# Performance work log

Measured on AMD Instinct MI355X. Metric: run time of the kernel, lower is better.

Reference implementation:

```python
import jax, jax.numpy as jnp
import numpy as np

B, HI, WI, DIM = 16, 64, 64, 256
HEADS, HEAD_DIM, NUM_MEM = 8, 32, 4
HID = HEADS * HEAD_DIM


def setup_inputs() -> dict:
    key = jax.random.key(0)
    ks = jax.random.split(key, 6)
    return {
        "x": jax.random.normal(ks[0], (B, HI, WI, DIM), jnp.float32),
        "gamma_in": jax.random.normal(ks[1], (DIM,), jnp.float32) * 0.02,
        "w_qkv": jax.random.normal(ks[2], (DIM, 3 * HID), jnp.float32) / np.sqrt(DIM),
        "b_qkv": jnp.zeros((3 * HID,), jnp.float32),
        "mem_kv": jax.random.normal(ks[3], (2, HEADS, NUM_MEM, HEAD_DIM), jnp.float32),
        "w_out": jax.random.normal(ks[4], (HID, DIM), jnp.float32) / np.sqrt(HID),
        "b_out": jnp.zeros((DIM,), jnp.float32),
        "gamma_out": jax.random.normal(ks[5], (DIM,), jnp.float32) * 0.02,
    }


def reference(x, gamma_in, w_qkv, b_qkv, mem_kv, w_out, b_out, gamma_out):
    b, h, w, c = x.shape
    n = h * w
    rms_scale = c ** 0.5
    attn_scale = HEAD_DIM ** -0.5

    # RMSNorm (as written in source: pure learned scaling)
    xn = x * (gamma_in + 1.0) * rms_scale

    # 1x1 conv == per-pixel linear projection
    qkv = xn @ w_qkv + b_qkv                       # (b, h, w, 3*HID)
    q, k, v = jnp.split(qkv, 3, axis=-1)

    def to_heads(t):                                # (b,h,w,HID) -> (b, heads, d, n)
        return t.reshape(b, n, HEADS, HEAD_DIM).transpose(0, 2, 3, 1)

    q, k, v = map(to_heads, (q, k, v))

    # memory kv: (heads, m, d) -> (b, heads, d, m), concat along sequence axis
    mk = jnp.broadcast_to(mem_kv[0].transpose(0, 2, 1)[None], (b, HEADS, HEAD_DIM, NUM_MEM))
    mv = jnp.broadcast_to(mem_kv[1].transpose(0, 2, 1)[None], (b, HEADS, HEAD_DIM, NUM_MEM))
    k = jnp.concatenate([mk, k], axis=-1)           # (b, heads, d, n+m)
    v = jnp.concatenate([mv, v], axis=-1)

    # feature-map attention: softmax q over feature dim, k over sequence dim
    q = jax.nn.softmax(q * attn_scale, axis=-2)     # source scales q before softmax
    k = jax.nn.softmax(k, axis=-1)

    context = jnp.einsum('bhdn,bhen->bhde', k, v)   # (b, heads, d, e) small
    out = jnp.einsum('bhde,bhdn->bhen', context, q) # (b, heads, e, n)

    out = out.transpose(0, 3, 1, 2).reshape(b, h, w, HID)
    y = out @ w_out + b_out                         # 1x1 output conv
    return y * (gamma_out + 1.0) * rms_scale        # output RMSNorm
```

## Files before the change

kernel.cpp:

```cpp
#include <hip/hip_runtime.h>
#include <hip/hip_bf16.h>

typedef __bf16 bf16_t;
typedef _Float16 fp16_t;
typedef _Float16 f16x8 __attribute__((ext_vector_type(8)));
typedef __bf16 bf16x8 __attribute__((ext_vector_type(8)));
typedef __bf16 bf16x4 __attribute__((ext_vector_type(4)));
typedef float f32x4 __attribute__((ext_vector_type(4)));

#define ATTN_SCALE 0.17677669529663687f
#define K_SHIFT 64.0f
#define Q_SHIFT 8.0f

__device__ __forceinline__ void gload16(const void* g, void* l) {
  __builtin_amdgcn_global_load_lds((const __attribute__((address_space(1))) void*)g,
                                   (__attribute__((address_space(3))) void*)l, 16, 0, 0);
}

__global__ __launch_bounds__(256) void prep_pack(
    const float* __restrict__ w_qkv, fp16_t* __restrict__ Bpack) {
  int idx = blockIdx.x * 256 + threadIdx.x;
  int l = idx & 63;
  int rest = idx >> 6;
  int f = rest & 3;
  int kk = (rest >> 2) & 7;
  int nt = rest >> 5;
  int n = nt * 64 + f * 16 + (l & 15);
  int k0 = kk * 32 + (l >> 4) * 8;
  f16x8 v;
#pragma unroll
  for (int e = 0; e < 8; ++e) v[e] = (fp16_t)w_qkv[(k0 + e) * 768 + n];
  ((f16x8*)Bpack)[idx] = v;
}

__global__ __launch_bounds__(256) void gemm_qvk_ctx(
    const float* __restrict__ x, const float* __restrict__ gamma_in,
    const fp16_t* __restrict__ Bpack, const float* __restrict__ bias,
    fp16_t* __restrict__ qe_out, float* __restrict__ part) {
  __shared__ fp16_t A[64 * 256];
  __shared__ bf16_t Pl[64 * 64];
  __shared__ bf16_t Vl[64 * 64];
  int t = threadIdx.x, l = t & 63, w = t >> 6;
  int lr = l >> 4, lc = l & 15;
  int bx = blockIdx.x;
  int m0 = bx * 64;

#pragma unroll
  for (int i = 0; i < 8; ++i) {
    int idx = i * 256 + t;
    int r = idx >> 5, c8 = idx & 31;
    const float* src = x + (size_t)(m0 + r) * 256 + c8 * 8;
    const float* gsc = gamma_in + c8 * 8;
    f16x8 hv;
#pragma unroll
    for (int j = 0; j < 8; ++j) hv[j] = (fp16_t)(src[j] * (gsc[j] + 1.f) * 16.f);
    *(f16x8*)&A[r * 256 + ((c8 ^ (r & 31)) * 8)] = hv;
  }
  __syncthreads();

  {
    const fp16_t* Bp = Bpack + (size_t)w * 16384;
    f32x4 acc[4][4];
#pragma unroll
    for (int mf = 0; mf < 4; ++mf)
#pragma unroll
      for (int nf = 0; nf < 4; ++nf) acc[mf][nf] = (f32x4){0.f, 0.f, 0.f, 0.f};
#pragma unroll
    for (int kk = 0; kk < 8; ++kk) {
      f16x8 af[4], bfr[4];
#pragma unroll
      for (int f = 0; f < 4; ++f) {
        int ra = f * 16 + lc;
        af[f] = *(const f16x8*)&A[ra * 256 + (((kk * 4 + lr) ^ (ra & 31)) * 8)];
        bfr[f] = *(const f16x8*)(Bp + (size_t)(kk * 4 + f) * 512 + l * 8);
      }
#pragma unroll
      for (int mf = 0; mf < 4; ++mf)
#pragma unroll
        for (int nf = 0; nf < 4; ++nf)
          acc[mf][nf] = __builtin_amdgcn_mfma_f32_16x16x32_f16(af[mf], bfr[nf], acc[mf][nf], 0, 0, 0);
    }
    int n0 = w * 64;
    float bq[4];
#pragma unroll
    for (int nf = 0; nf < 4; ++nf) bq[nf] = bias[n0 + nf * 16 + lc];
#pragma unroll
    for (int mf = 0; mf < 4; ++mf)
#pragma unroll
      for (int r = 0; r < 4; ++r) {
        int row = m0 + mf * 16 + lr * 4 + r;
#pragma unroll
        for (int nf = 0; nf < 4; ++nf) {
          float ql = (acc[mf][nf][r] + bq[nf]) * ATTN_SCALE;
          qe_out[(size_t)row * 256 + n0 + nf * 16 + lc] = (fp16_t)__expf(ql - Q_SHIFT);
        }
      }
  }

  bool isK = (w < 2);
  int rh = w & 1;
  int hq = w & 1;
  int chalf = w >> 1;
  for (int ph = 0; ph < 4; ++ph) {
    int nt = (isK ? 4 : 8) + ph;
    const fp16_t* Bp = Bpack + (size_t)nt * 16384;
    f32x4 acc[2][4];
#pragma unroll
    for (int mf = 0; mf < 2; ++mf)
#pragma unroll
      for (int nf = 0; nf < 4; ++nf) acc[mf][nf] = (f32x4){0.f, 0.f, 0.f, 0.f};
#pragma unroll
    for (int kk = 0; kk < 8; ++kk) {
      f16x8 af[2], bfr[4];
#pragma unroll
      for (int f = 0; f < 2; ++f) {
        int ra = rh * 32 + f * 16 + lc;
        af[f] = *(const f16x8*)&A[ra * 256 + (((kk * 4 + lr) ^ (ra & 31)) * 8)];
      }
#pragma unroll
      for (int f = 0; f < 4; ++f)
        bfr[f] = *(const f16x8*)(Bp + (size_t)(kk * 4 + f) * 512 + l * 8);
#pragma unroll
      for (int mf = 0; mf < 2; ++mf)
#pragma unroll
        for (int nf = 0; nf < 4; ++nf)
          acc[mf][nf] = __builtin_amdgcn_mfma_f32_16x16x32_f16(af[mf], bfr[nf], acc[mf][nf], 0, 0, 0);
    }
    int n0 = nt * 64;
    float bv[4];
#pragma unroll
    for (int nf = 0; nf < 4; ++nf) bv[nf] = bias[n0 + nf * 16 + lc];
#pragma unroll
    for (int mf = 0; mf < 2; ++mf) {
#pragma unroll
      for (int nf = 0; nf < 4; ++nf) {
        int col = nf * 16 + lc;
        int row0 = rh * 32 + mf * 16 + lr * 4;
        bf16x4 pk;
#pragma unroll
        for (int r = 0; r < 4; ++r) {
          float val = acc[mf][nf][r] + bv[nf];
          pk[r] = isK ? (bf16_t)__expf(val - K_SHIFT) : (bf16_t)val;
        }
        int addr = col * 64 + ((((row0 >> 3) ^ (col & 7)) << 3) | (row0 & 7));
        if (isK) *(bf16x4*)&Pl[addr] = pk;
        else     *(bf16x4*)&Vl[addr] = pk;
      }
    }
    __syncthreads();

    {
      int hb = hq * 32;
      f32x4 sacc[2];
      f32x4 zacc[2];
#pragma unroll
      for (int mf = 0; mf < 2; ++mf) {
        sacc[mf] = (f32x4){0.f, 0.f, 0.f, 0.f};
        zacc[mf] = (f32x4){0.f, 0.f, 0.f, 0.f};
      }
      bf16x8 ones;
#pragma unroll
      for (int i = 0; i < 8; ++i) ones[i] = (bf16_t)1.0f;
#pragma unroll
      for (int kk = 0; kk < 2; ++kk) {
        bf16x8 ap[2], bvv;
#pragma unroll
        for (int mf = 0; mf < 2; ++mf) {
          int colA = hb + mf * 16 + lc;
          ap[mf] = *(const bf16x8*)&Pl[colA * 64 + (((kk * 4 + lr) ^ (colA & 7)) << 3)];
        }
        int colB = hb + chalf * 16 + lc;
        bvv = *(const bf16x8*)&Vl[colB * 64 + (((kk * 4 + lr) ^ (colB & 7)) << 3)];
#pragma unroll
        for (int mf = 0; mf < 2; ++mf) {
          sacc[mf] = __builtin_amdgcn_mfma_f32_16x16x32_bf16(ap[mf], bvv, sacc[mf], 0, 0, 0);
          if (chalf == 0)
            zacc[mf] = __builtin_amdgcn_mfma_f32_16x16x32_bf16(ap[mf], ones, zacc[mf], 0, 0, 0);
        }
      }
      float* pp = part + (size_t)bx * 8448 + (ph * 2 + hq) * 1056;
#pragma unroll
      for (int mf = 0; mf < 2; ++mf)
#pragma unroll
        for (int r = 0; r < 4; ++r) {
          int dd = mf * 16 + lr * 4 + r;
          pp[dd * 32 + chalf * 16 + lc] = sacc[mf][r];
          if (chalf == 0 && lc == 0) pp[1024 + dd] = zacc[mf][r];
        }
    }
    __syncthreads();
  }
}

__global__ __launch_bounds__(256) void build_wt(
    const float* __restrict__ part, const float* __restrict__ w_out,
    const float* __restrict__ mem_kv, fp16_t* __restrict__ Bpacky) {
  int bh = blockIdx.x;
  int b = bh >> 3, h = bh & 7;
  int t = threadIdx.x;
  __shared__ float S[32][32];
  __shared__ float Zr[32];
  __shared__ float W[32][256];
  for (int idx = t; idx < 1024; idx += 256) {
    float s = 0.f;
    for (int c = 0; c < 64; ++c) s += part[((size_t)(b * 64 + c)) * 8448 + h * 1056 + idx];
    S[idx >> 5][idx & 31] = s;
  }
  if (t < 32) {
    float zz = 0.f;
    for (int c = 0; c < 64; ++c) zz += part[((size_t)(b * 64 + c)) * 8448 + h * 1056 + 1024 + t];
    Zr[t] = zz;
  }
  for (int i = t; i < 32 * 256; i += 256) W[i >> 8][i & 255] = w_out[(h * 32 + (i >> 8)) * 256 + (i & 255)];
  __syncthreads();
  if (t < 32) {
    int dd = t;
    for (int m = 0; m < 4; ++m) {
      float p = __expf(mem_kv[h * 128 + m * 32 + dd] - K_SHIFT);
      Zr[dd] += p;
      for (int e = 0; e < 32; ++e) S[dd][e] += p * mem_kv[1024 + h * 128 + m * 32 + e];
    }
  }
  __syncthreads();
  int c = t;
  int nt = c >> 6, f = (c >> 4) & 3, lc = c & 15;
  for (int dd = 0; dd < 32; ++dd) {
    float acc = 0;
#pragma unroll 8
    for (int e = 0; e < 32; ++e) acc += S[dd][e] * W[e][c];
    int kcol = h * 32 + dd;
    int kk = kcol >> 5, lr = (kcol & 31) >> 3, e8 = kcol & 7;
    size_t addr = ((((size_t)(b * 4 + nt) * 8 + kk) * 4 + f) * 64 + (lr * 16 + lc)) * 8 + e8;
    Bpacky[addr] = (fp16_t)(acc / Zr[dd]);
  }
}

__global__ __launch_bounds__(256) void gemm_y(
    const fp16_t* __restrict__ qe, const fp16_t* __restrict__ Bpacky,
    const float* __restrict__ b_out, const float* __restrict__ gamma_out,
    float* __restrict__ y_out) {
  __shared__ fp16_t A[64 * 256];
  __shared__ float zbuf[64][8];
  int t = threadIdx.x, l = t & 63, w = t >> 6;
  int lr = l >> 4, lc = l & 15;
  int m0 = blockIdx.x * 64;
#pragma unroll
  for (int i = 0; i < 8; ++i) {
    int idx = i * 256 + t;
    int r = idx >> 5, cs = idx & 31;
    gload16(qe + (size_t)(m0 + r) * 256 + ((cs ^ (r & 31)) * 8), &A[idx * 8]);
  }
  __syncthreads();

#pragma unroll
  for (int pi = 0; pi < 2; ++pi) {
    int p = pi * 256 + t;
    int r = p >> 3, hh = p & 7;
    float zs = 0.f;
#pragma unroll
    for (int c = 0; c < 4; ++c) {
      int cs = (hh * 4 + c) ^ (r & 31);
      f16x8 vv = *(const f16x8*)&A[r * 256 + cs * 8];
#pragma unroll
      for (int j = 0; j < 8; ++j) zs += (float)vv[j];
    }
    zbuf[r][hh] = 1.f / zs;
  }
  __syncthreads();

#pragma unroll
  for (int i = 0; i < 8; ++i) {
    int idx = i * 256 + t;
    int r = idx >> 5, cs = idx & 31;
    int hh = (cs ^ (r & 31)) >> 2;
    float sc = zbuf[r][hh];
    f16x8 vv = *(const f16x8*)&A[idx * 8];
#pragma unroll
    for (int j = 0; j < 8; ++j) vv[j] = (fp16_t)((float)vv[j] * sc);
    *(f16x8*)&A[idx * 8] = vv;
  }
  __syncthreads();

  int n0 = w * 64;
  const fp16_t* Bp = Bpacky + (size_t)(m0 >> 12) * 65536 + (size_t)w * 16384;
  f32x4 acc[4][4];
#pragma unroll
  for (int mf = 0; mf < 4; ++mf)
#pragma unroll
    for (int nf = 0; nf < 4; ++nf) acc[mf][nf] = (f32x4){0.f, 0.f, 0.f, 0.f};
#pragma unroll
  for (int kk = 0; kk < 8; ++kk) {
    f16x8 af[4], bfr[4];
#pragma unroll
    for (int f = 0; f < 4; ++f) {
      int ra = f * 16 + lc;
      af[f] = *(const f16x8*)&A[ra * 256 + (((kk * 4 + lr) ^ (ra & 31)) * 8)];
      bfr[f] = *(const f16x8*)(Bp + (size_t)(kk * 4 + f) * 512 + l * 8);
    }
#pragma unroll
    for (int mf = 0; mf < 4; ++mf)
#pragma unroll
      for (int nf = 0; nf < 4; ++nf)
        acc[mf][nf] = __builtin_amdgcn_mfma_f32_16x16x32_f16(af[mf], bfr[nf], acc[mf][nf], 0, 0, 0);
  }
  float bv[4], gv[4];
#pragma unroll
  for (int nf = 0; nf < 4; ++nf) {
    int c = n0 + nf * 16 + lc;
    bv[nf] = b_out[c];
    gv[nf] = (gamma_out[c] + 1.f) * 16.f;
  }
#pragma unroll
  for (int mf = 0; mf < 4; ++mf)
#pragma unroll
    for (int r = 0; r < 4; ++r) {
      int row = m0 + mf * 16 + lr * 4 + r;
#pragma unroll
      for (int nf = 0; nf < 4; ++nf)
        y_out[(size_t)row * 256 + n0 + nf * 16 + lc] = (acc[mf][nf][r] + bv[nf]) * gv[nf];
    }
}

extern "C" void kernel_launch(void* const* d_in, const int* in_sizes, int n_in,
                              void* d_out, int out_size, void* d_ws, size_t ws_size,
                              hipStream_t stream) {
  const float* x        = (const float*)d_in[0];
  const float* gamma_in = (const float*)d_in[1];
  const float* w_qkv    = (const float*)d_in[2];
  const float* b_qkv    = (const float*)d_in[3];
  const float* mem_kv   = (const float*)d_in[4];
  const float* w_out    = (const float*)d_in[5];
  const float* b_out    = (const float*)d_in[6];
  const float* gamma_out= (const float*)d_in[7];
  float* y = (float*)d_out;

  char* ws = (char*)d_ws;
  fp16_t* qe     = (fp16_t*)(ws);
  fp16_t* Bpack  = (fp16_t*)(ws + 33554432);
  fp16_t* Bpacky = (fp16_t*)(ws + 33947648);
  float*  part   = (float*)(ws + 36044800);

  prep_pack<<<96, 256, 0, stream>>>(w_qkv, Bpack);
  gemm_qvk_ctx<<<1024, 256, 0, stream>>>(x, gamma_in, Bpack, b_qkv, qe, part);
  build_wt<<<128, 256, 0, stream>>>(part, w_out, mem_kv, Bpacky);
  gemm_y<<<1024, 256, 0, stream>>>(qe, Bpacky, b_out, gamma_out, y);
}
```

Before: 128.1 us.

## Recompute Q projection in output GEMM instead of storing exp(q) intermediate

Moves the Q projection out of the KV/context kernel into the final output kernel. There it recomputes Q from x, applies a proper per-head softmax with wave shuffles, and feeds the result straight from LDS into the y GEMM. This removes the 32 MB fp16 qe write and read round trip and the separate normalization passes. The cost is reading x twice, once in each kernel, plus redoing the Q GEMM in the second kernel.

```diff
diff --git a/kernel.cpp b/kernel.cpp
--- a/kernel.cpp
+++ b/kernel.cpp
@@ -10,7 +10,6 @@
 
 #define ATTN_SCALE 0.17677669529663687f
 #define K_SHIFT 64.0f
-#define Q_SHIFT 8.0f
 
 __device__ __forceinline__ void gload16(const void* g, void* l) {
   __builtin_amdgcn_global_load_lds((const __attribute__((address_space(1))) void*)g,
@@ -33,10 +32,10 @@
   ((f16x8*)Bpack)[idx] = v;
 }
 
-__global__ __launch_bounds__(256) void gemm_qvk_ctx(
+__global__ __launch_bounds__(256) void gemm_kv_ctx(
     const float* __restrict__ x, const float* __restrict__ gamma_in,
     const fp16_t* __restrict__ Bpack, const float* __restrict__ bias,
-    fp16_t* __restrict__ qe_out, float* __restrict__ part) {
+    float* __restrict__ part) {
   __shared__ fp16_t A[64 * 256];
   __shared__ bf16_t Pl[64 * 64];
   __shared__ bf16_t Vl[64 * 64];
@@ -57,45 +56,6 @@
     *(f16x8*)&A[r * 256 + ((c8 ^ (r & 31)) * 8)] = hv;
   }
   __syncthreads();
-
-  {
-    const fp16_t* Bp = Bpack + (size_t)w * 16384;
-    f32x4 acc[4][4];
-#pragma unroll
-    for (int mf = 0; mf < 4; ++mf)
-#pragma unroll
-      for (int nf = 0; nf < 4; ++nf) acc[mf][nf] = (f32x4){0.f, 0.f, 0.f, 0.f};
-#pragma unroll
-    for (int kk = 0; kk < 8; ++kk) {
-      f16x8 af[4], bfr[4];
-#pragma unroll
-      for (int f = 0; f < 4; ++f) {
-        int ra = f * 16 + lc;
-        af[f] = *(const f16x8*)&A[ra * 256 + (((kk * 4 + lr) ^ (ra & 31)) * 8)];
-        bfr[f] = *(const f16x8*)(Bp + (size_t)(kk * 4 + f) * 512 + l * 8);
-      }
-#pragma unroll
-      for (int mf = 0; mf < 4; ++mf)
-#pragma unroll
-        for (int nf = 0; nf < 4; ++nf)
-          acc[mf][nf] = __builtin_amdgcn_mfma_f32_16x16x32_f16(af[mf], bfr[nf], acc[mf][nf], 0, 0, 0);
-    }
-    int n0 = w * 64;
-    float bq[4];
-#pragma unroll
-    for (int nf = 0; nf < 4; ++nf) bq[nf] = bias[n0 + nf * 16 + lc];
-#pragma unroll
-    for (int mf = 0; mf < 4; ++mf)
-#pragma unroll
-      for (int r = 0; r < 4; ++r) {
-        int row = m0 + mf * 16 + lr * 4 + r;
-#pragma unroll
-        for (int nf = 0; nf < 4; ++nf) {
-          float ql = (acc[mf][nf][r] + bq[nf]) * ATTN_SCALE;
-          qe_out[(size_t)row * 256 + n0 + nf * 16 + lc] = (fp16_t)__expf(ql - Q_SHIFT);
-        }
-      }
-  }
 
   bool isK = (w < 2);
   int rh = w & 1;
@@ -235,55 +195,97 @@
   }
 }
 
-__global__ __launch_bounds__(256) void gemm_y(
-    const fp16_t* __restrict__ qe, const fp16_t* __restrict__ Bpacky,
+__global__ __launch_bounds__(256) void gemm_qy(
+    const float* __restrict__ x, const float* __restrict__ gamma_in,
+    const fp16_t* __restrict__ Bpack, const float* __restrict__ bias,
+    const fp16_t* __restrict__ Bpacky,
     const float* __restrict__ b_out, const float* __restrict__ gamma_out,
     float* __restrict__ y_out) {
   __shared__ fp16_t A[64 * 256];
-  __shared__ float zbuf[64][8];
   int t = threadIdx.x, l = t & 63, w = t >> 6;
   int lr = l >> 4, lc = l & 15;
   int m0 = blockIdx.x * 64;
+
 #pragma unroll
   for (int i = 0; i < 8; ++i) {
     int idx = i * 256 + t;
-    int r = idx >> 5, cs = idx & 31;
-    gload16(qe + (size_t)(m0 + r) * 256 + ((cs ^ (r & 31)) * 8), &A[idx * 8]);
-  }
-  __syncthreads();
-
-#pragma unroll
-  for (int pi = 0; pi < 2; ++pi) {
-    int p = pi * 256 + t;
-    int r = p >> 3, hh = p & 7;
-    float zs = 0.f;
-#pragma unroll
-    for (int c = 0; c < 4; ++c) {
-      int cs = (hh * 4 + c) ^ (r & 31);
-      f16x8 vv = *(const f16x8*)&A[r * 256 + cs * 8];
-#pragma unroll
-      for (int j = 0; j < 8; ++j) zs += (float)vv[j];
-    }
-    zbuf[r][hh] = 1.f / zs;
-  }
-  __syncthreads();
-
-#pragma unroll
-  for (int i = 0; i < 8; ++i) {
-    int idx = i * 256 + t;
-    int r = idx >> 5, cs = idx & 31;
-    int hh = (cs ^ (r & 31)) >> 2;
-    float sc = zbuf[r][hh];
-    f16x8 vv = *(const f16x8*)&A[idx * 8];
-#pragma unroll
-    for (int j = 0; j < 8; ++j) vv[j] = (fp16_t)((float)vv[j] * sc);
-    *(f16x8*)&A[idx * 8] = vv;
-  }
-  __syncthreads();
-
-  int n0 = w * 64;
+    int r = idx >> 5, c8 = idx & 31;
+    const float* src = x + (size_t)(m0 + r) * 256 + c8 * 8;
+    const float* gsc = gamma_in + c8 * 8;
+    f16x8 hv;
+#pragma unroll
+    for (int j = 0; j < 8; ++j) hv[j] = (fp16_t)(src[j] * (gsc[j] + 1.f) * 16.f);
+    *(f16x8*)&A[r * 256 + ((c8 ^ (r & 31)) * 8)] = hv;
+  }
+  __syncthreads();
+
+  f32x4 acc[4][4];
+#pragma unroll
+  for (int mf = 0; mf < 4; ++mf)
+#pragma unroll
+    for (int nf = 0; nf < 4; ++nf) acc[mf][nf] = (f32x4){0.f, 0.f, 0.f, 0.f};
+  {
+    const fp16_t* Bp = Bpack + (size_t)w * 16384;
+#pragma unroll
+    for (int kk = 0; kk < 8; ++kk) {
+      f16x8 af[4], bfr[4];
+#pragma unroll
+      for (int f = 0; f < 4; ++f) {
+        int ra = f * 16 + lc;
+        af[f] = *(const f16x8*)&A[ra * 256 + (((kk * 4 + lr) ^ (ra & 31)) * 8)];
+        bfr[f] = *(const f16x8*)(Bp + (size_t)(kk * 4 + f) * 512 + l * 8);
+      }
+#pragma unroll
+      for (int mf = 0; mf < 4; ++mf)
+#pragma unroll
+        for (int nf = 0; nf < 4; ++nf)
+          acc[mf][nf] = __builtin_amdgcn_mfma_f32_16x16x32_f16(af[mf], bfr[nf], acc[mf][nf], 0, 0, 0);
+    }
+  }
+  __syncthreads();
+
+  {
+    int n0 = w * 64;
+    float bq[4];
+#pragma unroll
+    for (int nf = 0; nf < 4; ++nf) bq[nf] = bias[n0 + nf * 16 + lc];
+#pragma unroll
+    for (int mf = 0; mf < 4; ++mf) {
+#pragma unroll
+      for (int r = 0; r < 4; ++r) {
+        int row = mf * 16 + lr * 4 + r;
+        float v0 = (acc[mf][0][r] + bq[0]) * ATTN_SCALE;
+        float v1 = (acc[mf][1][r] + bq[1]) * ATTN_SCALE;
+        float v2 = (acc[mf][2][r] + bq[2]) * ATTN_SCALE;
+        float v3 = (acc[mf][3][r] + bq[3]) * ATTN_SCALE;
+        float mA = fmaxf(v0, v1), mB = fmaxf(v2, v3);
+#pragma unroll
+        for (int s = 1; s < 16; s <<= 1) {
+          mA = fmaxf(mA, __shfl_xor(mA, s));
+          mB = fmaxf(mB, __shfl_xor(mB, s));
+        }
+        float e0 = __expf(v0 - mA), e1 = __expf(v1 - mA);
+        float e2 = __expf(v2 - mB), e3 = __expf(v3 - mB);
+        float sA = e0 + e1, sB = e2 + e3;
+#pragma unroll
+        for (int s = 1; s < 16; s <<= 1) {
+          sA += __shfl_xor(sA, s);
+          sB += __shfl_xor(sB, s);
+        }
+        float rA = 1.f / sA, rB = 1.f / sB;
+        float qv[4] = {e0 * rA, e1 * rA, e2 * rB, e3 * rB};
+#pragma unroll
+        for (int nf = 0; nf < 4; ++nf) {
+          int col = n0 + nf * 16 + lc;
+          int c8 = col >> 3;
+          A[row * 256 + ((c8 ^ (row & 31)) * 8) + (col & 7)] = (fp16_t)qv[nf];
+        }
+      }
+    }
+  }
+  __syncthreads();
+
   const fp16_t* Bp = Bpacky + (size_t)(m0 >> 12) * 65536 + (size_t)w * 16384;
-  f32x4 acc[4][4];
 #pragma unroll
   for (int mf = 0; mf < 4; ++mf)
 #pragma unroll
@@ -303,6 +305,7 @@
       for (int nf = 0; nf < 4; ++nf)
         acc[mf][nf] = __builtin_amdgcn_mfma_f32_16x16x32_f16(af[mf], bfr[nf], acc[mf][nf], 0, 0, 0);
   }
+  int n0 = w * 64;
   float bv[4], gv[4];
 #pragma unroll
   for (int nf = 0; nf < 4; ++nf) {
@@ -335,13 +338,12 @@
   float* y = (float*)d_out;
 
   char* ws = (char*)d_ws;
-  fp16_t* qe     = (fp16_t*)(ws);
-  fp16_t* Bpack  = (fp16_t*)(ws + 33554432);
-  fp16_t* Bpacky = (fp16_t*)(ws + 33947648);
-  float*  part   = (float*)(ws + 36044800);
+  fp16_t* Bpack  = (fp16_t*)(ws);
+  fp16_t* Bpacky = (fp16_t*)(ws + 393216);
+  float*  part   = (float*)(ws + 2490368);
 
   prep_pack<<<96, 256, 0, stream>>>(w_qkv, Bpack);
-  gemm_qvk_ctx<<<1024, 256, 0, stream>>>(x, gamma_in, Bpack, b_qkv, qe, part);
+  gemm_kv_ctx<<<1024, 256, 0, stream>>>(x, gamma_in, Bpack, b_qkv, part);
   build_wt<<<128, 256, 0, stream>>>(part, w_out, mem_kv, Bpacky);
-  gemm_y<<<1024, 256, 0, stream>>>(qe, Bpacky, b_out, gamma_out, y);
-}
+  gemm_qy<<<1024, 256, 0, stream>>>(x, gamma_in, Bpack, b_qkv, Bpacky, b_out, gamma_out, y);
+}
```

Measured after the change: 137.4 us. +7.3%, slower.
